# Kernel tuning notes

Hardware: AMD Instinct MI355X
Metric: run time of the kernel (lower is better)

The kernel has to match this reference:

```python
import jax, jax.numpy as jnp
import numpy as np

B, T, D, H, OUT = 256, 256, 300, 200, 100


def setup_inputs() -> dict:
    key = jax.random.key(0)
    ks = jax.random.split(key, 8)
    s = 0.05
    x = jax.random.normal(ks[0], (B, T, D), jnp.float32)
    lengths = jax.random.randint(ks[1], (B,), 1, T + 1, jnp.int32)
    return {
        "x": x,
        "lengths": lengths,
        "Wx_f": jax.random.normal(ks[2], (D, 3 * H), jnp.float32) * s,
        "Wh_f": jax.random.normal(ks[3], (H, 3 * H), jnp.float32) * s,
        "bx_f": jnp.zeros((3 * H,), jnp.float32),
        "bh_f": jnp.zeros((3 * H,), jnp.float32),
        "Wx_b": jax.random.normal(ks[4], (D, 3 * H), jnp.float32) * s,
        "Wh_b": jax.random.normal(ks[5], (H, 3 * H), jnp.float32) * s,
        "bx_b": jnp.zeros((3 * H,), jnp.float32),
        "bh_b": jnp.zeros((3 * H,), jnp.float32),
        "Wd": jax.random.normal(ks[6], (2 * H, OUT), jnp.float32) * s,
        "bd": jnp.zeros((OUT,), jnp.float32),
    }


def _gru_scan(x_proj, Wh, bh, mask):
    """x_proj: [T,B,3H] precomputed x@Wx+bx; mask: [T,B,1] bool (valid step).
    Keras GRU, reset_after=True, gate order [z, r, h]."""
    h0 = jnp.zeros((x_proj.shape[1], Wh.shape[0]), x_proj.dtype)

    def step(h, inp):
        xp, m = inp
        rec = h @ Wh + bh  # [B,3H]
        xz, xr, xh = jnp.split(xp, 3, axis=-1)
        rz, rr, rh = jnp.split(rec, 3, axis=-1)
        z = jax.nn.sigmoid(xz + rz)
        r = jax.nn.sigmoid(xr + rr)
        hh = jnp.tanh(xh + r * rh)
        h_new = z * h + (1.0 - z) * hh
        h_new = jnp.where(m, h_new, h)  # freeze state on padding
        return h_new, h_new

    _, hs = jax.lax.scan(step, h0, (x_proj, mask))
    return hs  # [T,B,H]


def reference(x, lengths, Wx_f, Wh_f, bx_f, bh_f, Wx_b, Wh_b, bx_b, bh_b, Wd, bd):
    Bsz, Ts, _ = x.shape
    t_idx = jnp.arange(Ts)
    valid = t_idx[None, :] < lengths[:, None]          # [B,T]
    mask = valid.T[:, :, None]                          # [T,B,1]

    # forward direction
    xp_f = (x @ Wx_f + bx_f).transpose(1, 0, 2)         # [T,B,3H]
    hs_f = _gru_scan(xp_f, Wh_f, bh_f, mask)

    # backward direction: reverse each sequence within its valid length
    rev_idx = jnp.clip(lengths[:, None] - 1 - t_idx[None, :], 0)  # [B,T]
    x_rev = jnp.take_along_axis(x, rev_idx[:, :, None], axis=1)
    xp_b = (x_rev @ Wx_b + bx_b).transpose(1, 0, 2)
    hs_b = _gru_scan(xp_b, Wh_b, bh_b, mask)

    m = mask.astype(x.dtype)
    sum_f = jnp.sum(hs_f * m, axis=0)                   # [B,H]
    sum_b = jnp.sum(hs_b * m, axis=0)                   # [B,H]
    L = lengths.astype(x.dtype)[:, None]
    # original: reduce_mean over time (/L) then extra / x[i].shape[0] (/L)
    pooled = jnp.concatenate([sum_f, sum_b], axis=-1) / (L * L)  # [B,2H]
    return jnp.tanh(pooled @ Wd + bd)                   # [B,100]
```

## Files before the change

kernel.cpp:

```cpp
#include <hip/hip_runtime.h>
#include <hip/hip_fp16.h>
#include <stdint.h>

typedef _Float16 f16;
typedef _Float16 f16x8 __attribute__((ext_vector_type(8)));
typedef _Float16 f16x4 __attribute__((ext_vector_type(4)));
typedef _Float16 f16x2 __attribute__((ext_vector_type(2)));
typedef float f32x4 __attribute__((ext_vector_type(4)));
typedef uint32_t u32x4 __attribute__((ext_vector_type(4)));

#define NB 256
#define NT 256
#define ND 300
#define NH 200
#define NOUT 100
#define C3H 600
#define NTILE 40
#define NKCX 10
#define NKCH 7
#define WHT 48
#define SLABF 9984
#define SLABB 19968
#define LOG2E 1.44269504088896f

#define XP_BYTES   (2ull * NT * 16 * SLABB)
#define WXP_BYTES  (2ull * NKCX * NTILE * 512 * 2)
#define WHP_BYTES  (2ull * NKCH * WHT * 512 * 2)

typedef const __attribute__((address_space(1))) uint32_t ga_u32;
typedef __attribute__((address_space(3))) uint32_t lds_u32;

__device__ __forceinline__ float fast_exp2(float x) {
#if __has_builtin(__builtin_amdgcn_exp2f)
  return __builtin_amdgcn_exp2f(x);
#else
  return exp2f(x);
#endif
}
__device__ __forceinline__ float fast_rcp(float x) {
#if __has_builtin(__builtin_amdgcn_rcpf)
  return __builtin_amdgcn_rcpf(x);
#else
  return 1.f / x;
#endif
}

__global__ void pack_w(const float* __restrict__ Wxf, const float* __restrict__ Wxb,
                       const float* __restrict__ Whf, const float* __restrict__ Whb,
                       f16* __restrict__ wxp, f16* __restrict__ whp) {
  int e = blockIdx.x * 256 + threadIdx.x;
  const int NX = 2 * NKCX * NTILE * 512;
  const int NHW = 2 * NKCH * WHT * 512;
  if (e < NX) {
    int j = e & 7, lane = (e >> 3) & 63;
    int tile = (e >> 9) % NTILE;
    int kc = ((e >> 9) / NTILE) % NKCX;
    int dir = (e >> 9) / (NTILE * NKCX);
    int k = kc * 32 + ((lane >> 4) * 8) + j;
    int c = lane & 15;
    float v = 0.f;
    if (tile < 39) {
      int s = tile / 13, ii = tile % 13;
      int hc = ii * 16 + c;
      if (k < ND && hc < NH) {
        const float* W = dir ? Wxb : Wxf;
        float sc = (s == 2) ? 2.f * LOG2E : -LOG2E;
        v = W[k * C3H + s * NH + hc] * sc;
      }
    }
    wxp[e] = (f16)v;
  } else if (e < NX + NHW) {
    int e2 = e - NX;
    int j = e2 & 7, lane = (e2 >> 3) & 63;
    int tile = (e2 >> 9) % WHT;
    int kc = ((e2 >> 9) / WHT) % NKCH;
    int dir = (e2 >> 9) / (WHT * NKCH);
    int tp = tile / 3, s = tile % 3;
    int k = kc * 32 + ((lane >> 4) * 8) + j;
    int c = lane & 15;
    float v = 0.f;
    if (tp < 13) {
      int hc = tp * 16 + c;
      if (k < NH && hc < NH) {
        const float* W = dir ? Whb : Whf;
        float sc = (s == 2) ? 2.f * LOG2E : -LOG2E;
        v = W[k * C3H + s * NH + hc] * sc;
      }
    }
    whp[e2] = (f16)v;
  }
}

__global__ __launch_bounds__(512, 2) void xproj(
    const float* __restrict__ x, const int* __restrict__ len,
    const f16* __restrict__ wxp,
    const float* __restrict__ bxf, const float* __restrict__ bxb,
    const float* __restrict__ bhf, const float* __restrict__ bhb,
    f16* __restrict__ xp) {
  __shared__ f16 As[128 * 328];
  __shared__ f16 Bs[NTILE * 512];
  int blk = blockIdx.x;
  int dir = blk >> 9;
  int m0 = (blk & 511) * 128;
  int t = m0 >> 8;
  int bstart = m0 & 255;
  int tid = threadIdx.x;
  int lane = tid & 63, w = tid >> 6;

  {
    int r = tid >> 2, q = tid & 3;
    int b = bstart + r;
    int srct = t;
    if (dir) { int L = len[b]; srct = L - 1 - t; if (srct < 0) srct = 0; }
    const float* xrow = x + ((size_t)b * NT + srct) * ND;
#pragma unroll
    for (int s = 0; s < 20; ++s) {
      int i4 = q + 4 * s;
      f16x4 h4;
      if (i4 < 75) {
        float4 v = *(const float4*)(xrow + 4 * i4);
        h4 = (f16x4){(f16)v.x, (f16)v.y, (f16)v.z, (f16)v.w};
      } else {
        h4 = (f16x4){(f16)0.f, (f16)0.f, (f16)0.f, (f16)0.f};
      }
      *(f16x4*)(&As[r * 328 + 4 * i4]) = h4;
    }
  }

  f32x4 acc[8][5];
#pragma unroll
  for (int rt = 0; rt < 8; ++rt)
#pragma unroll
    for (int i = 0; i < 5; ++i) acc[rt][i] = (f32x4){0.f, 0.f, 0.f, 0.f};

  const f16* wxp_d = wxp + (size_t)dir * NKCX * NTILE * 512;
  for (int kc = 0; kc < NKCX; ++kc) {
#pragma unroll
    for (int i = 0; i < 5; ++i) {
      int idx = w + 8 * i;
      const f16* src = wxp_d + ((size_t)kc * NTILE + idx) * 512 + lane * 8;
      __builtin_amdgcn_global_load_lds((ga_u32*)src, (lds_u32*)(&Bs[idx * 512]), 16, 0, 0);
    }
    __syncthreads();
#pragma unroll
    for (int rt = 0; rt < 8; ++rt) {
      f16x8 af = *(const f16x8*)(&As[(rt * 16 + (lane & 15)) * 328 + kc * 32 + (lane >> 4) * 8]);
#pragma unroll
      for (int i = 0; i < 5; ++i) {
        f16x8 bf = *(const f16x8*)(&Bs[(5 * w + i) * 512 + lane * 8]);
        acc[rt][i] = __builtin_amdgcn_mfma_f32_16x16x32_f16(af, bf, acc[rt][i], 0, 0, 0);
      }
    }
    __syncthreads();
  }

  const float* bx = dir ? bxb : bxf;
  const float* bh = dir ? bhb : bhf;
  int c = lane & 15;
#pragma unroll
  for (int i = 0; i < 5; ++i) {
    int tile = 5 * w + i;
    if (tile >= 39) continue;
    int s = tile / 13, ii = tile % 13;
    int hc = ii * 16 + c;
    float addv = 0.f;
    if (hc < NH) {
      int col600 = s * NH + hc;
      float sc = (s == 2) ? 2.f * LOG2E : -LOG2E;
      addv = (bx[col600] + (s < 2 ? bh[col600] : 0.f)) * sc;
    }
#pragma unroll
    for (int rt = 0; rt < 8; ++rt) {
      int bg = (bstart >> 4) + rt;
      f16* dst = xp + (((size_t)dir * NT + t) * 16 + bg) * SLABF + ((ii * 3 + s) * 64 + lane) * 4;
      f16x4 v4 = {(f16)(acc[rt][i][0] + addv), (f16)(acc[rt][i][1] + addv),
                  (f16)(acc[rt][i][2] + addv), (f16)(acc[rt][i][3] + addv)};
      *(f16x4*)dst = v4;
    }
  }
}

__global__ __launch_bounds__(512)
__attribute__((amdgpu_waves_per_eu(2, 2)))
void birnn(
    const f16* __restrict__ xp, const f16* __restrict__ whp,
    const int* __restrict__ len,
    const float* __restrict__ bhf, const float* __restrict__ bhb,
    float* __restrict__ sums) {
  __shared__ f16 hls[2][16 * 232];
  __shared__ __align__(16) f16 xpl[2][10240];
  int blk = blockIdx.x;
  int dir = blk >> 4;
  int b0 = (blk & 15) << 4;
  int tid = threadIdx.x;
  int lane = tid & 63, w = tid >> 6;
  int g = lane >> 4, c = lane & 15;

  u32x4 whu[2][3][7];
  const f16* whp_d = whp + (size_t)dir * NKCH * WHT * 512;
#pragma unroll
  for (int tp = 0; tp < 2; ++tp) {
    int trip = tp ? (w + 8) : w;
#pragma unroll
    for (int s = 0; s < 3; ++s)
#pragma unroll
      for (int kc = 0; kc < NKCH; ++kc)
        whu[tp][s][kc] = *(const u32x4*)(whp_d + ((size_t)(kc * WHT + trip * 3 + s)) * 512 + lane * 8);
  }
#pragma unroll
  for (int tp = 0; tp < 2; ++tp)
#pragma unroll
    for (int s = 0; s < 3; ++s)
#pragma unroll
      for (int kc = 0; kc < NKCH; ++kc)
        asm volatile("" : "+v"(whu[tp][s][kc]));

  for (int o = tid; o < 2 * 16 * 232; o += 512) ((f16*)hls)[o] = (f16)0.f;

  int len4[4];
#pragma unroll
  for (int jj = 0; jj < 4; ++jj) len4[jj] = len[b0 + g * 4 + jj];
  int maxlen = 0;
  for (int i = 0; i < 16; ++i) { int L = len[b0 + i]; maxlen = L > maxlen ? L : maxlen; }

  const float* bh = dir ? bhb : bhf;
  float bhh[2] = {0.f, 0.f};
  f32x4 hreg[2] = {(f32x4){0.f,0.f,0.f,0.f}, (f32x4){0.f,0.f,0.f,0.f}};
  f32x4 sum[2] = {(f32x4){0.f,0.f,0.f,0.f}, (f32x4){0.f,0.f,0.f,0.f}};
#pragma unroll
  for (int tp = 0; tp < 2; ++tp) {
    int ii = tp ? (w + 8) : w;
    int hc = ii * 16 + c;
    if (ii < 13 && hc < NH) bhh[tp] = bh[2 * NH + hc] * (2.f * LOG2E);
  }

  const char* slab0 = (const char*)(xp) + (((size_t)dir * NT) * 16 + (b0 >> 4)) * (size_t)SLABB;
  const size_t slab_stride = (size_t)16 * SLABB;

  if (w >= 5) {
    int o0 = (w - 5) * 7, o1 = (w == 7) ? 20 : o0 + 7;
    const char* src = slab0;
    for (int k = o0; k < o1; ++k)
      __builtin_amdgcn_global_load_lds((ga_u32*)(src + k * 1024 + lane * 16),
                                       (lds_u32*)((char*)(&xpl[0][0]) + k * 1024), 16, 0, 0);
  }
  __syncthreads();

  for (int t = 0; t < maxlen; ++t) {
    int cur = t & 1, nxt = cur ^ 1;
    if (w >= 5 && (t + 1) < maxlen) {
      int o0 = (w - 5) * 7, o1 = (w == 7) ? 20 : o0 + 7;
      const char* src = slab0 + (size_t)(t + 1) * slab_stride;
      for (int k = o0; k < o1; ++k)
        __builtin_amdgcn_global_load_lds((ga_u32*)(src + k * 1024 + lane * 16),
                                         (lds_u32*)((char*)(&xpl[nxt][0]) + k * 1024), 16, 0, 0);
    }

    f32x4 acc[2][3];
#pragma unroll
    for (int tp = 0; tp < 2; ++tp)
#pragma unroll
      for (int s = 0; s < 3; ++s) acc[tp][s] = (f32x4){0.f, 0.f, 0.f, 0.f};
#pragma unroll
    for (int kc = 0; kc < NKCH; ++kc) {
      f16x8 a = *(const f16x8*)(&hls[cur][c * 232 + kc * 32 + g * 8]);
#pragma unroll
      for (int tp = 0; tp < 2; ++tp)
#pragma unroll
        for (int s = 0; s < 3; ++s)
          acc[tp][s] = __builtin_amdgcn_mfma_f32_16x16x32_f16(
              a, __builtin_bit_cast(f16x8, whu[tp][s][kc]), acc[tp][s], 0, 0, 0);
    }

#pragma unroll
    for (int tp = 0; tp < 2; ++tp) {
      int ii = tp ? (w + 8) : w;
      if (ii < 13) {
        f16x4 xz4 = *(const f16x4*)(&xpl[cur][((ii * 3 + 0) * 64 + lane) * 4]);
        f16x4 xr4 = *(const f16x4*)(&xpl[cur][((ii * 3 + 1) * 64 + lane) * 4]);
        f16x4 xh4 = *(const f16x4*)(&xpl[cur][((ii * 3 + 2) * 64 + lane) * 4]);
#pragma unroll
        for (int jj = 0; jj < 4; ++jj) {
          float az = (float)xz4[jj] + acc[tp][0][jj];
          float z  = fast_rcp(1.f + fast_exp2(az));
          float ar = (float)xr4[jj] + acc[tp][1][jj];
          float r  = fast_rcp(1.f + fast_exp2(ar));
          float c2 = fmaf(r, acc[tp][2][jj] + bhh[tp], (float)xh4[jj]);
          float q2 = fast_rcp(1.f + fast_exp2(c2));
          float th = fmaf(-2.f, q2, 1.f);
          float hold = hreg[tp][jj];
          float hn = fmaf(z, hold - th, th);
          bool va = (t < len4[jj]);
          hn = va ? hn : hold;
          hreg[tp][jj] = hn;
          sum[tp][jj] += va ? hn : 0.f;
        }
        int hc = ii * 16 + c;
        if (hc < NH) {
          f16x2 plo = __builtin_bit_cast(f16x2, __builtin_amdgcn_cvt_pkrtz(hreg[tp][0], hreg[tp][1]));
          f16x2 phi = __builtin_bit_cast(f16x2, __builtin_amdgcn_cvt_pkrtz(hreg[tp][2], hreg[tp][3]));
          hls[nxt][(g * 4 + 0) * 232 + hc] = plo[0];
          hls[nxt][(g * 4 + 1) * 232 + hc] = plo[1];
          hls[nxt][(g * 4 + 2) * 232 + hc] = phi[0];
          hls[nxt][(g * 4 + 3) * 232 + hc] = phi[1];
        }
      }
    }
    __syncthreads();
  }

#pragma unroll
  for (int tp = 0; tp < 2; ++tp) {
    int ii = tp ? (w + 8) : w;
    int hc = ii * 16 + c;
    if (ii < 13 && hc < NH) {
#pragma unroll
      for (int jj = 0; jj < 4; ++jj)
        sums[((size_t)dir * NB + b0 + g * 4 + jj) * NH + hc] = sum[tp][jj];
    }
  }
}

__global__ void head_k(const float* __restrict__ sums, const int* __restrict__ len,
                       const float* __restrict__ Wd, const float* __restrict__ bd,
                       float* __restrict__ out) {
  __shared__ float pl[2 * NH];
  int b = blockIdx.x, tid = threadIdx.x;
  float L = (float)len[b];
  float inv = 1.f / (L * L);
  for (int k = tid; k < 2 * NH; k += 128) {
    int d = k < NH ? 0 : 1;
    int j = k < NH ? k : k - NH;
    pl[k] = sums[((size_t)d * NB + b) * NH + j] * inv;
  }
  __syncthreads();
  if (tid < NOUT) {
    float a = bd[tid];
    for (int k = 0; k < 2 * NH; ++k) a = fmaf(pl[k], Wd[k * NOUT + tid], a);
    out[b * NOUT + tid] = tanhf(a);
  }
}

extern "C" void kernel_launch(void* const* d_in, const int* in_sizes, int n_in,
                              void* d_out, int out_size, void* d_ws, size_t ws_size,
                              hipStream_t stream) {
  const float* x   = (const float*)d_in[0];
  const int*   len = (const int*)d_in[1];
  const float* Wxf = (const float*)d_in[2];
  const float* Whf = (const float*)d_in[3];
  const float* bxf = (const float*)d_in[4];
  const float* bhf = (const float*)d_in[5];
  const float* Wxb = (const float*)d_in[6];
  const float* Whb = (const float*)d_in[7];
  const float* bxb = (const float*)d_in[8];
  const float* bhb = (const float*)d_in[9];
  const float* Wd  = (const float*)d_in[10];
  const float* bd  = (const float*)d_in[11];
  float* out = (float*)d_out;
  char* ws = (char*)d_ws;
  f16* xp  = (f16*)(ws);
  f16* wxp = (f16*)(ws + XP_BYTES + 1024);
  f16* whp = (f16*)(ws + XP_BYTES + 1024 + WXP_BYTES);
  float* sums = (float*)(ws + XP_BYTES + 1024 + WXP_BYTES + WHP_BYTES);

  hipLaunchKernelGGL(pack_w, dim3(2944), dim3(256), 0, stream,
                     Wxf, Wxb, Whf, Whb, wxp, whp);
  hipLaunchKernelGGL(xproj, dim3(1024), dim3(512), 0, stream,
                     x, len, wxp, bxf, bxb, bhf, bhb, xp);
  hipLaunchKernelGGL(birnn, dim3(32), dim3(512), 0, stream,
                     xp, whp, len, bhf, bhb, sums);
  hipLaunchKernelGGL(head_k, dim3(256), dim3(128), 0, stream,
                     sums, len, Wd, bd, out);
}
```

Measured before the change: 623.8 us.

## Spread GRU recurrence over 13 waves, trim K tail, widen xproj blocks

The recurrent kernel now runs 13 waves per block, one 16-column hidden tile each, instead of 8 waves that each handled two tiles. This shortens the serial per-step MFMA and gate chain that bounds the latency of the recurrence. The LDS double-buffered prefetch of x-projections is replaced by direct per-lane global loads. The K tail (192..199) uses a 16x16x16 MFMA so the last chunk does less padded work, and the hidden state is kept in fp16 registers. xproj moves to 1024-thread blocks with a 2x8 wave grid, which halves accumulators per thread but may cost occupancy, and the direct global loads sit on the serial path with no prefetch.

```diff
diff --git a/kernel.cpp b/kernel.cpp
--- a/kernel.cpp
+++ b/kernel.cpp
@@ -5,9 +5,10 @@
 typedef _Float16 f16;
 typedef _Float16 f16x8 __attribute__((ext_vector_type(8)));
 typedef _Float16 f16x4 __attribute__((ext_vector_type(4)));
-typedef _Float16 f16x2 __attribute__((ext_vector_type(2)));
+typedef __fp16 h16x4 __attribute__((ext_vector_type(4)));
 typedef float f32x4 __attribute__((ext_vector_type(4)));
 typedef uint32_t u32x4 __attribute__((ext_vector_type(4)));
+typedef uint32_t u32x2 __attribute__((ext_vector_type(2)));
 
 #define NB 256
 #define NT 256
@@ -29,6 +30,12 @@
 
 typedef const __attribute__((address_space(1))) uint32_t ga_u32;
 typedef __attribute__((address_space(3))) uint32_t lds_u32;
+
+#if __has_builtin(__builtin_amdgcn_mfma_f32_16x16x16f16)
+#define TAIL16 1
+#else
+#define TAIL16 0
+#endif
 
 __device__ __forceinline__ float fast_exp2(float x) {
 #if __has_builtin(__builtin_amdgcn_exp2f)
@@ -76,12 +83,25 @@
     int kc = ((e2 >> 9) / WHT) % NKCH;
     int dir = (e2 >> 9) / (WHT * NKCH);
     int tp = tile / 3, s = tile % 3;
-    int k = kc * 32 + ((lane >> 4) * 8) + j;
     int c = lane & 15;
+    int k;
+    bool kvalid;
+    if (kc < 6) {
+      k = kc * 32 + ((lane >> 4) * 8) + j;
+      kvalid = true;
+    } else {
+#if TAIL16
+      k = 192 + ((lane >> 4) * 4) + j;
+      kvalid = (j < 4) && (k < NH);
+#else
+      k = 192 + ((lane >> 4) * 8) + j;
+      kvalid = (k < NH);
+#endif
+    }
     float v = 0.f;
     if (tp < 13) {
       int hc = tp * 16 + c;
-      if (k < NH && hc < NH) {
+      if (kvalid && hc < NH) {
         const float* W = dir ? Whb : Whf;
         float sc = (s == 2) ? 2.f * LOG2E : -LOG2E;
         v = W[k * C3H + s * NH + hc] * sc;
@@ -91,7 +111,7 @@
   }
 }
 
-__global__ __launch_bounds__(512, 2) void xproj(
+__global__ __launch_bounds__(1024) void xproj(
     const float* __restrict__ x, const int* __restrict__ len,
     const f16* __restrict__ wxp,
     const float* __restrict__ bxf, const float* __restrict__ bxb,
@@ -106,16 +126,18 @@
   int bstart = m0 & 255;
   int tid = threadIdx.x;
   int lane = tid & 63, w = tid >> 6;
+  int g = lane >> 4, c = lane & 15;
+  int rh = w >> 3, cg = w & 7;
 
   {
-    int r = tid >> 2, q = tid & 3;
+    int r = tid >> 3, q = tid & 7;
     int b = bstart + r;
     int srct = t;
     if (dir) { int L = len[b]; srct = L - 1 - t; if (srct < 0) srct = 0; }
     const float* xrow = x + ((size_t)b * NT + srct) * ND;
 #pragma unroll
-    for (int s = 0; s < 20; ++s) {
-      int i4 = q + 4 * s;
+    for (int s = 0; s < 10; ++s) {
+      int i4 = q + 8 * s;
       f16x4 h4;
       if (i4 < 75) {
         float4 v = *(const float4*)(xrow + 4 * i4);
@@ -127,27 +149,29 @@
     }
   }
 
-  f32x4 acc[8][5];
-#pragma unroll
-  for (int rt = 0; rt < 8; ++rt)
+  f32x4 acc[4][5];
+#pragma unroll
+  for (int rt = 0; rt < 4; ++rt)
 #pragma unroll
     for (int i = 0; i < 5; ++i) acc[rt][i] = (f32x4){0.f, 0.f, 0.f, 0.f};
 
   const f16* wxp_d = wxp + (size_t)dir * NKCX * NTILE * 512;
   for (int kc = 0; kc < NKCX; ++kc) {
 #pragma unroll
-    for (int i = 0; i < 5; ++i) {
-      int idx = w + 8 * i;
-      const f16* src = wxp_d + ((size_t)kc * NTILE + idx) * 512 + lane * 8;
-      __builtin_amdgcn_global_load_lds((ga_u32*)src, (lds_u32*)(&Bs[idx * 512]), 16, 0, 0);
+    for (int i = 0; i < 3; ++i) {
+      int idx = w + 16 * i;
+      if (idx < NTILE) {
+        const f16* src = wxp_d + ((size_t)kc * NTILE + idx) * 512 + lane * 8;
+        __builtin_amdgcn_global_load_lds((ga_u32*)src, (lds_u32*)(&Bs[idx * 512]), 16, 0, 0);
+      }
     }
     __syncthreads();
 #pragma unroll
-    for (int rt = 0; rt < 8; ++rt) {
-      f16x8 af = *(const f16x8*)(&As[(rt * 16 + (lane & 15)) * 328 + kc * 32 + (lane >> 4) * 8]);
+    for (int rt = 0; rt < 4; ++rt) {
+      f16x8 af = *(const f16x8*)(&As[((rh * 4 + rt) * 16 + c) * 328 + kc * 32 + g * 8]);
 #pragma unroll
       for (int i = 0; i < 5; ++i) {
-        f16x8 bf = *(const f16x8*)(&Bs[(5 * w + i) * 512 + lane * 8]);
+        f16x8 bf = *(const f16x8*)(&Bs[(cg * 5 + i) * 512 + lane * 8]);
         acc[rt][i] = __builtin_amdgcn_mfma_f32_16x16x32_f16(af, bf, acc[rt][i], 0, 0, 0);
       }
     }
@@ -156,10 +180,9 @@
 
   const float* bx = dir ? bxb : bxf;
   const float* bh = dir ? bhb : bhf;
-  int c = lane & 15;
 #pragma unroll
   for (int i = 0; i < 5; ++i) {
-    int tile = 5 * w + i;
+    int tile = cg * 5 + i;
     if (tile >= 39) continue;
     int s = tile / 13, ii = tile % 13;
     int hc = ii * 16 + c;
@@ -170,8 +193,8 @@
       addv = (bx[col600] + (s < 2 ? bh[col600] : 0.f)) * sc;
     }
 #pragma unroll
-    for (int rt = 0; rt < 8; ++rt) {
-      int bg = (bstart >> 4) + rt;
+    for (int rt = 0; rt < 4; ++rt) {
+      int bg = (bstart >> 4) + rh * 4 + rt;
       f16* dst = xp + (((size_t)dir * NT + t) * 16 + bg) * SLABF + ((ii * 3 + s) * 64 + lane) * 4;
       f16x4 v4 = {(f16)(acc[rt][i][0] + addv), (f16)(acc[rt][i][1] + addv),
                   (f16)(acc[rt][i][2] + addv), (f16)(acc[rt][i][3] + addv)};
@@ -180,144 +203,130 @@
   }
 }
 
-__global__ __launch_bounds__(512)
-__attribute__((amdgpu_waves_per_eu(2, 2)))
-void birnn(
+__global__ __launch_bounds__(832) void birnn(
     const f16* __restrict__ xp, const f16* __restrict__ whp,
     const int* __restrict__ len,
     const float* __restrict__ bhf, const float* __restrict__ bhb,
     float* __restrict__ sums) {
   __shared__ f16 hls[2][16 * 232];
-  __shared__ __align__(16) f16 xpl[2][10240];
   int blk = blockIdx.x;
   int dir = blk >> 4;
   int b0 = (blk & 15) << 4;
   int tid = threadIdx.x;
   int lane = tid & 63, w = tid >> 6;
   int g = lane >> 4, c = lane & 15;
-
-  u32x4 whu[2][3][7];
+  int hc = w * 16 + c;
+
+  u32x4 whu[3][6];
+#if TAIL16
+  u32x2 wht[3];
+#else
+  u32x4 wht[3];
+#endif
   const f16* whp_d = whp + (size_t)dir * NKCH * WHT * 512;
 #pragma unroll
-  for (int tp = 0; tp < 2; ++tp) {
-    int trip = tp ? (w + 8) : w;
-#pragma unroll
-    for (int s = 0; s < 3; ++s)
-#pragma unroll
-      for (int kc = 0; kc < NKCH; ++kc)
-        whu[tp][s][kc] = *(const u32x4*)(whp_d + ((size_t)(kc * WHT + trip * 3 + s)) * 512 + lane * 8);
-  }
-#pragma unroll
-  for (int tp = 0; tp < 2; ++tp)
-#pragma unroll
-    for (int s = 0; s < 3; ++s)
-#pragma unroll
-      for (int kc = 0; kc < NKCH; ++kc)
-        asm volatile("" : "+v"(whu[tp][s][kc]));
-
-  for (int o = tid; o < 2 * 16 * 232; o += 512) ((f16*)hls)[o] = (f16)0.f;
-
-  int len4[4];
-#pragma unroll
-  for (int jj = 0; jj < 4; ++jj) len4[jj] = len[b0 + g * 4 + jj];
+  for (int s = 0; s < 3; ++s) {
+#pragma unroll
+    for (int kc = 0; kc < 6; ++kc)
+      whu[s][kc] = *(const u32x4*)(whp_d + ((size_t)(kc * WHT + w * 3 + s)) * 512 + lane * 8);
+#if TAIL16
+    wht[s] = *(const u32x2*)(whp_d + ((size_t)(6 * WHT + w * 3 + s)) * 512 + lane * 8);
+#else
+    wht[s] = *(const u32x4*)(whp_d + ((size_t)(6 * WHT + w * 3 + s)) * 512 + lane * 8);
+#endif
+  }
+#pragma unroll
+  for (int s = 0; s < 3; ++s) {
+#pragma unroll
+    for (int kc = 0; kc < 6; ++kc) asm volatile("" : "+v"(whu[s][kc]));
+    asm volatile("" : "+v"(wht[s]));
+  }
+
+  for (int o = tid; o < 2 * 16 * 232; o += 832) ((f16*)hls)[o] = (f16)0.f;
+
+  int lenpack = 0;
+#pragma unroll
+  for (int jj = 0; jj < 4; ++jj) lenpack |= (len[b0 + g * 4 + jj] - 1) << (8 * jj);
   int maxlen = 0;
   for (int i = 0; i < 16; ++i) { int L = len[b0 + i]; maxlen = L > maxlen ? L : maxlen; }
 
   const float* bh = dir ? bhb : bhf;
-  float bhh[2] = {0.f, 0.f};
-  f32x4 hreg[2] = {(f32x4){0.f,0.f,0.f,0.f}, (f32x4){0.f,0.f,0.f,0.f}};
-  f32x4 sum[2] = {(f32x4){0.f,0.f,0.f,0.f}, (f32x4){0.f,0.f,0.f,0.f}};
-#pragma unroll
-  for (int tp = 0; tp < 2; ++tp) {
-    int ii = tp ? (w + 8) : w;
-    int hc = ii * 16 + c;
-    if (ii < 13 && hc < NH) bhh[tp] = bh[2 * NH + hc] * (2.f * LOG2E);
-  }
-
-  const char* slab0 = (const char*)(xp) + (((size_t)dir * NT) * 16 + (b0 >> 4)) * (size_t)SLABB;
-  const size_t slab_stride = (size_t)16 * SLABB;
-
-  if (w >= 5) {
-    int o0 = (w - 5) * 7, o1 = (w == 7) ? 20 : o0 + 7;
-    const char* src = slab0;
-    for (int k = o0; k < o1; ++k)
-      __builtin_amdgcn_global_load_lds((ga_u32*)(src + k * 1024 + lane * 16),
-                                       (lds_u32*)((char*)(&xpl[0][0]) + k * 1024), 16, 0, 0);
-  }
+  float bhh = (hc < NH) ? bh[2 * NH + hc] * (2.f * LOG2E) : 0.f;
+  f16x4 hreg = {};
+  f32x4 sum = {(f32x4){0.f, 0.f, 0.f, 0.f}};
+
+  const char* xrow = (const char*)xp
+      + (((size_t)dir * NT) * 16 + (size_t)(blk & 15)) * (size_t)SLABB
+      + (size_t)(w * 3) * 512 + (size_t)lane * 8;
+
   __syncthreads();
 
   for (int t = 0; t < maxlen; ++t) {
     int cur = t & 1, nxt = cur ^ 1;
-    if (w >= 5 && (t + 1) < maxlen) {
-      int o0 = (w - 5) * 7, o1 = (w == 7) ? 20 : o0 + 7;
-      const char* src = slab0 + (size_t)(t + 1) * slab_stride;
-      for (int k = o0; k < o1; ++k)
-        __builtin_amdgcn_global_load_lds((ga_u32*)(src + k * 1024 + lane * 16),
-                                         (lds_u32*)((char*)(&xpl[nxt][0]) + k * 1024), 16, 0, 0);
-    }
-
-    f32x4 acc[2][3];
-#pragma unroll
-    for (int tp = 0; tp < 2; ++tp)
-#pragma unroll
-      for (int s = 0; s < 3; ++s) acc[tp][s] = (f32x4){0.f, 0.f, 0.f, 0.f};
-#pragma unroll
-    for (int kc = 0; kc < NKCH; ++kc) {
-      f16x8 a = *(const f16x8*)(&hls[cur][c * 232 + kc * 32 + g * 8]);
-#pragma unroll
-      for (int tp = 0; tp < 2; ++tp)
-#pragma unroll
-        for (int s = 0; s < 3; ++s)
-          acc[tp][s] = __builtin_amdgcn_mfma_f32_16x16x32_f16(
-              a, __builtin_bit_cast(f16x8, whu[tp][s][kc]), acc[tp][s], 0, 0, 0);
-    }
-
-#pragma unroll
-    for (int tp = 0; tp < 2; ++tp) {
-      int ii = tp ? (w + 8) : w;
-      if (ii < 13) {
-        f16x4 xz4 = *(const f16x4*)(&xpl[cur][((ii * 3 + 0) * 64 + lane) * 4]);
-        f16x4 xr4 = *(const f16x4*)(&xpl[cur][((ii * 3 + 1) * 64 + lane) * 4]);
-        f16x4 xh4 = *(const f16x4*)(&xpl[cur][((ii * 3 + 2) * 64 + lane) * 4]);
-#pragma unroll
-        for (int jj = 0; jj < 4; ++jj) {
-          float az = (float)xz4[jj] + acc[tp][0][jj];
-          float z  = fast_rcp(1.f + fast_exp2(az));
-          float ar = (float)xr4[jj] + acc[tp][1][jj];
-          float r  = fast_rcp(1.f + fast_exp2(ar));
-          float c2 = fmaf(r, acc[tp][2][jj] + bhh[tp], (float)xh4[jj]);
-          float q2 = fast_rcp(1.f + fast_exp2(c2));
-          float th = fmaf(-2.f, q2, 1.f);
-          float hold = hreg[tp][jj];
-          float hn = fmaf(z, hold - th, th);
-          bool va = (t < len4[jj]);
-          hn = va ? hn : hold;
-          hreg[tp][jj] = hn;
-          sum[tp][jj] += va ? hn : 0.f;
-        }
-        int hc = ii * 16 + c;
-        if (hc < NH) {
-          f16x2 plo = __builtin_bit_cast(f16x2, __builtin_amdgcn_cvt_pkrtz(hreg[tp][0], hreg[tp][1]));
-          f16x2 phi = __builtin_bit_cast(f16x2, __builtin_amdgcn_cvt_pkrtz(hreg[tp][2], hreg[tp][3]));
-          hls[nxt][(g * 4 + 0) * 232 + hc] = plo[0];
-          hls[nxt][(g * 4 + 1) * 232 + hc] = plo[1];
-          hls[nxt][(g * 4 + 2) * 232 + hc] = phi[0];
-          hls[nxt][(g * 4 + 3) * 232 + hc] = phi[1];
-        }
-      }
+    u32x2 xzv = *(const u32x2*)(xrow);
+    u32x2 xrv = *(const u32x2*)(xrow + 512);
+    u32x2 xhv = *(const u32x2*)(xrow + 1024);
+    xrow += (size_t)16 * SLABB;
+
+    f32x4 a0 = {0.f,0.f,0.f,0.f}, a1 = {0.f,0.f,0.f,0.f}, a2 = {0.f,0.f,0.f,0.f};
+    const f16* hb = &hls[cur][c * 232 + g * 8];
+#pragma unroll
+    for (int kc = 0; kc < 6; ++kc) {
+      f16x8 af = *(const f16x8*)(hb + kc * 32);
+      a0 = __builtin_amdgcn_mfma_f32_16x16x32_f16(af, __builtin_bit_cast(f16x8, whu[0][kc]), a0, 0, 0, 0);
+      a1 = __builtin_amdgcn_mfma_f32_16x16x32_f16(af, __builtin_bit_cast(f16x8, whu[1][kc]), a1, 0, 0, 0);
+      a2 = __builtin_amdgcn_mfma_f32_16x16x32_f16(af, __builtin_bit_cast(f16x8, whu[2][kc]), a2, 0, 0, 0);
+    }
+#if TAIL16
+    {
+      h16x4 at = *(const h16x4*)(&hls[cur][c * 232 + 192 + g * 4]);
+      a0 = __builtin_amdgcn_mfma_f32_16x16x16f16(at, __builtin_bit_cast(h16x4, wht[0]), a0, 0, 0, 0);
+      a1 = __builtin_amdgcn_mfma_f32_16x16x16f16(at, __builtin_bit_cast(h16x4, wht[1]), a1, 0, 0, 0);
+      a2 = __builtin_amdgcn_mfma_f32_16x16x16f16(at, __builtin_bit_cast(h16x4, wht[2]), a2, 0, 0, 0);
+    }
+#else
+    {
+      f16x8 at = *(const f16x8*)(&hls[cur][c * 232 + 192 + g * 8]);
+      a0 = __builtin_amdgcn_mfma_f32_16x16x32_f16(at, __builtin_bit_cast(f16x8, wht[0]), a0, 0, 0, 0);
+      a1 = __builtin_amdgcn_mfma_f32_16x16x32_f16(at, __builtin_bit_cast(f16x8, wht[1]), a1, 0, 0, 0);
+      a2 = __builtin_amdgcn_mfma_f32_16x16x32_f16(at, __builtin_bit_cast(f16x8, wht[2]), a2, 0, 0, 0);
+    }
+#endif
+
+    if (hc < NH) {
+      f16x4 xz4 = __builtin_bit_cast(f16x4, xzv);
+      f16x4 xr4 = __builtin_bit_cast(f16x4, xrv);
+      f16x4 xh4 = __builtin_bit_cast(f16x4, xhv);
+      float hn[4];
+#pragma unroll
+      for (int jj = 0; jj < 4; ++jj) {
+        float az = (float)xz4[jj] + a0[jj];
+        float z  = fast_rcp(1.f + fast_exp2(az));
+        float ar = (float)xr4[jj] + a1[jj];
+        float r  = fast_rcp(1.f + fast_exp2(ar));
+        float c2 = fmaf(r, a2[jj] + bhh, (float)xh4[jj]);
+        float th = fmaf(-2.f, fast_rcp(1.f + fast_exp2(c2)), 1.f);
+        float hold = (float)hreg[jj];
+        float v = fmaf(z, hold - th, th);
+        bool va = t <= ((lenpack >> (8 * jj)) & 255);
+        v = va ? v : hold;
+        sum[jj] += va ? v : 0.f;
+        hn[jj] = v;
+      }
+      uint32_t plo = __builtin_bit_cast(uint32_t, __builtin_amdgcn_cvt_pkrtz(hn[0], hn[1]));
+      uint32_t phi = __builtin_bit_cast(uint32_t, __builtin_amdgcn_cvt_pkrtz(hn[2], hn[3]));
+      hreg = __builtin_bit_cast(f16x4, (u32x2){plo, phi});
+#pragma unroll
+      for (int jj = 0; jj < 4; ++jj)
+        hls[nxt][(g * 4 + jj) * 232 + hc] = hreg[jj];
     }
     __syncthreads();
   }
 
-#pragma unroll
-  for (int tp = 0; tp < 2; ++tp) {
-    int ii = tp ? (w + 8) : w;
-    int hc = ii * 16 + c;
-    if (ii < 13 && hc < NH) {
-#pragma unroll
-      for (int jj = 0; jj < 4; ++jj)
-        sums[((size_t)dir * NB + b0 + g * 4 + jj) * NH + hc] = sum[tp][jj];
-    }
+  if (hc < NH) {
+#pragma unroll
+    for (int jj = 0; jj < 4; ++jj)
+      sums[((size_t)dir * NB + b0 + g * 4 + jj) * NH + hc] = sum[jj];
   }
 }
 
@@ -365,9 +374,9 @@
 
   hipLaunchKernelGGL(pack_w, dim3(2944), dim3(256), 0, stream,
                      Wxf, Wxb, Whf, Whb, wxp, whp);
-  hipLaunchKernelGGL(xproj, dim3(1024), dim3(512), 0, stream,
+  hipLaunchKernelGGL(xproj, dim3(1024), dim3(1024), 0, stream,
                      x, len, wxp, bxf, bxb, bhf, bhb, xp);
-  hipLaunchKernelGGL(birnn, dim3(32), dim3(512), 0, stream,
+  hipLaunchKernelGGL(birnn, dim3(32), dim3(832), 0, stream,
                      xp, whp, len, bhf, bhb, sums);
   hipLaunchKernelGGL(head_k, dim3(256), dim3(128), 0, stream,
                      sums, len, Wd, bd, out);
```

After: 658.8 us. 5.6% more time.
